# Performance work log

Measured on AMD Instinct MI355X. Metric: run time of the kernel, lower is better.

## Reference

```python
import jax, jax.numpy as jnp
import numpy as np

BATCH, DIM, ORDER = 16384, 1024, 3

def setup_inputs() -> dict:
    key = jax.random.key(0)
    k1, k2, k3 = jax.random.split(key, 3)
    x0 = jax.random.normal(k1, (BATCH, DIM), dtype=jnp.float32)
    # xavier-uniform init scale for w of shape (d, 1): sqrt(6/(d+1))
    limit = float(np.sqrt(6.0 / (DIM + 1)))
    W = jax.random.uniform(k2, (ORDER, DIM), dtype=jnp.float32, minval=-limit, maxval=limit)
    B = jnp.zeros((ORDER, DIM), dtype=jnp.float32)
    return {"x0": x0, "W": W, "B": B}

def reference(x0, W, B):
    # CrossLayer: xi_next = (x0 xi^T) w + b + xi == x0 * (xi . w) + b + xi
    # (outer product followed by matmul with w collapses to a dot-product scale)
    xi = x0
    for l in range(W.shape[0]):  # small fixed number of cross layers
        s = xi @ W[l]                      # [B]  dot(xi, w_l)
        xi = x0 * s[:, None] + B[l] + xi   # [B, D]
    return xi
```

## Files before the change

### kernel.cpp

```cpp
#include <hip/hip_runtime.h>


#define CN_BATCH 16384
#define CN_DIM   1024
#define CN_ORDER 3

__global__ __launch_bounds__(256) void
crossnet_kernel(const float* __restrict__ x0,
                const float* __restrict__ W,
                const float* __restrict__ B,
                float* __restrict__ out)
{
    const int tid  = threadIdx.x;
    const int wave = tid >> 6;
    const int lane = tid & 63;
    const int row  = blockIdx.x * 4 + wave;

    const float* __restrict__ xr = x0 + (size_t)row * CN_DIM;

    float4 x[4], xi[4];
#pragma unroll
    for (int c = 0; c < 4; ++c) {
        x[c]  = *reinterpret_cast<const float4*>(xr + c * 256 + lane * 4);
        xi[c] = x[c];
    }

#pragma unroll
    for (int l = 0; l < CN_ORDER; ++l) {
        const float* __restrict__ wl = W + l * CN_DIM;
        const float* __restrict__ bl = B + l * CN_DIM;

        float4 w[4];
#pragma unroll
        for (int c = 0; c < 4; ++c)
            w[c] = *reinterpret_cast<const float4*>(wl + c * 256 + lane * 4);

        float s = 0.f;
#pragma unroll
        for (int c = 0; c < 4; ++c) {
            s += xi[c].x * w[c].x;
            s += xi[c].y * w[c].y;
            s += xi[c].z * w[c].z;
            s += xi[c].w * w[c].w;
        }

#pragma unroll
        for (int off = 1; off < 64; off <<= 1)
            s += __shfl_xor(s, off, 64);

#pragma unroll
        for (int c = 0; c < 4; ++c) {
            const float4 b = *reinterpret_cast<const float4*>(bl + c * 256 + lane * 4);
            xi[c].x = fmaf(x[c].x, s, xi[c].x + b.x);
            xi[c].y = fmaf(x[c].y, s, xi[c].y + b.y);
            xi[c].z = fmaf(x[c].z, s, xi[c].z + b.z);
            xi[c].w = fmaf(x[c].w, s, xi[c].w + b.w);
        }
    }

    float* __restrict__ orow = out + (size_t)row * CN_DIM;
#pragma unroll
    for (int c = 0; c < 4; ++c)
        *reinterpret_cast<float4*>(orow + c * 256 + lane * 4) = xi[c];
}

extern "C" void kernel_launch(void* const* d_in, const int* in_sizes, int n_in,
                              void* d_out, int out_size, void* d_ws, size_t ws_size,
                              hipStream_t stream)
{
    const float* x0 = (const float*)d_in[0];
    const float* W  = (const float*)d_in[1];
    const float* B  = (const float*)d_in[2];
    float* out      = (float*)d_out;

    const int rows_per_block = 4;
    dim3 grid(CN_BATCH / rows_per_block);
    dim3 block(256);
    crossnet_kernel<<<grid, block, 0, stream>>>(x0, W, B, out);
}
```

Before: 120.5 us.

## Collapse cross layers into one scalar per row and pipeline multiple rows per wave

Uses the fact that every xi is x0 times a scalar plus an accumulated bias. That lets all three dot products be taken against x0 at once, with bias-weight dot products precomputed per block, and the output written as x0*cf + sum(B). Each wave now handles four rows and prefetches the next row while computing the current one. Loads and stores are nontemporal and the launch bound adds a min-blocks hint. The kernel is memory-bound, so the main gains would come from fewer serial reductions, less W/B traffic per row and better overlap, at the cost of higher register use.

```diff
diff --git a/kernel.cpp b/kernel.cpp
--- a/kernel.cpp
+++ b/kernel.cpp
@@ -3,9 +3,14 @@
 
 #define CN_BATCH 16384
 #define CN_DIM   1024
-#define CN_ORDER 3
 
-__global__ __launch_bounds__(256) void
+#define WAVES_PER_BLOCK 4
+#define ROWS_PER_WAVE   4
+#define ROWS_PER_BLOCK  (WAVES_PER_BLOCK * ROWS_PER_WAVE)
+
+typedef float f32x4 __attribute__((ext_vector_type(4)));
+
+__global__ __launch_bounds__(256, 4) void
 crossnet_kernel(const float* __restrict__ x0,
                 const float* __restrict__ W,
                 const float* __restrict__ B,
@@ -14,54 +19,88 @@
     const int tid  = threadIdx.x;
     const int wave = tid >> 6;
     const int lane = tid & 63;
-    const int row  = blockIdx.x * 4 + wave;
+    const int off0 = lane * 4;
 
-    const float* __restrict__ xr = x0 + (size_t)row * CN_DIM;
-
-    float4 x[4], xi[4];
+    f32x4 w0[4], w1[4], w2[4], bs[4];
+    float t1 = 0.f, t2 = 0.f;
 #pragma unroll
     for (int c = 0; c < 4; ++c) {
-        x[c]  = *reinterpret_cast<const float4*>(xr + c * 256 + lane * 4);
-        xi[c] = x[c];
+        const int off = c * 256 + off0;
+        w0[c] = *reinterpret_cast<const f32x4*>(W + 0 * CN_DIM + off);
+        w1[c] = *reinterpret_cast<const f32x4*>(W + 1 * CN_DIM + off);
+        w2[c] = *reinterpret_cast<const f32x4*>(W + 2 * CN_DIM + off);
+        const f32x4 b0 = *reinterpret_cast<const f32x4*>(B + 0 * CN_DIM + off);
+        const f32x4 b1 = *reinterpret_cast<const f32x4*>(B + 1 * CN_DIM + off);
+        const f32x4 b2 = *reinterpret_cast<const f32x4*>(B + 2 * CN_DIM + off);
+        bs[c] = b0 + b1 + b2;
+        t1 = fmaf(b0.x, w1[c].x, t1); t1 = fmaf(b0.y, w1[c].y, t1);
+        t1 = fmaf(b0.z, w1[c].z, t1); t1 = fmaf(b0.w, w1[c].w, t1);
+        t2 = fmaf(b0.x + b1.x, w2[c].x, t2); t2 = fmaf(b0.y + b1.y, w2[c].y, t2);
+        t2 = fmaf(b0.z + b1.z, w2[c].z, t2); t2 = fmaf(b0.w + b1.w, w2[c].w, t2);
+    }
+#pragma unroll
+    for (int o = 1; o < 64; o <<= 1) {
+        t1 += __shfl_xor(t1, o, 64);
+        t2 += __shfl_xor(t2, o, 64);
     }
 
+    const size_t row0 = ((size_t)blockIdx.x * WAVES_PER_BLOCK + wave) * ROWS_PER_WAVE;
+    const float* __restrict__ xr = x0 + row0 * (size_t)CN_DIM;
+
+    f32x4 cur[4], nxt[4];
 #pragma unroll
-    for (int l = 0; l < CN_ORDER; ++l) {
-        const float* __restrict__ wl = W + l * CN_DIM;
-        const float* __restrict__ bl = B + l * CN_DIM;
+    for (int c = 0; c < 4; ++c)
+        cur[c] = __builtin_nontemporal_load(
+            reinterpret_cast<const f32x4*>(xr + c * 256 + off0));
 
-        float4 w[4];
 #pragma unroll
-        for (int c = 0; c < 4; ++c)
-            w[c] = *reinterpret_cast<const float4*>(wl + c * 256 + lane * 4);
+    for (int r = 0; r < ROWS_PER_WAVE; ++r) {
+        if (r + 1 < ROWS_PER_WAVE) {
+#pragma unroll
+            for (int c = 0; c < 4; ++c)
+                nxt[c] = __builtin_nontemporal_load(
+                    reinterpret_cast<const f32x4*>(
+                        xr + (size_t)(r + 1) * CN_DIM + c * 256 + off0));
+        }
 
-        float s = 0.f;
+        float a0 = 0.f, a1 = 0.f, a2 = 0.f;
 #pragma unroll
         for (int c = 0; c < 4; ++c) {
-            s += xi[c].x * w[c].x;
-            s += xi[c].y * w[c].y;
-            s += xi[c].z * w[c].z;
-            s += xi[c].w * w[c].w;
+            a0 = fmaf(cur[c].x, w0[c].x, a0); a0 = fmaf(cur[c].y, w0[c].y, a0);
+            a0 = fmaf(cur[c].z, w0[c].z, a0); a0 = fmaf(cur[c].w, w0[c].w, a0);
+            a1 = fmaf(cur[c].x, w1[c].x, a1); a1 = fmaf(cur[c].y, w1[c].y, a1);
+            a1 = fmaf(cur[c].z, w1[c].z, a1); a1 = fmaf(cur[c].w, w1[c].w, a1);
+            a2 = fmaf(cur[c].x, w2[c].x, a2); a2 = fmaf(cur[c].y, w2[c].y, a2);
+            a2 = fmaf(cur[c].z, w2[c].z, a2); a2 = fmaf(cur[c].w, w2[c].w, a2);
         }
 
 #pragma unroll
-        for (int off = 1; off < 64; off <<= 1)
-            s += __shfl_xor(s, off, 64);
+        for (int o = 1; o < 64; o <<= 1) {
+            a0 += __shfl_xor(a0, o, 64);
+            a1 += __shfl_xor(a1, o, 64);
+            a2 += __shfl_xor(a2, o, 64);
+        }
+
+        const float s0 = a0;
+        const float s1 = fmaf(1.f + s0, a1, t1);
+        const float s2 = fmaf(1.f + s0 + s1, a2, t2);
+        const float cf = 1.f + s0 + s1 + s2;
+
+        float* __restrict__ orow = out + (row0 + (size_t)r) * CN_DIM;
+#pragma unroll
+        for (int c = 0; c < 4; ++c) {
+            f32x4 o;
+            o.x = fmaf(cur[c].x, cf, bs[c].x);
+            o.y = fmaf(cur[c].y, cf, bs[c].y);
+            o.z = fmaf(cur[c].z, cf, bs[c].z);
+            o.w = fmaf(cur[c].w, cf, bs[c].w);
+            __builtin_nontemporal_store(o,
+                reinterpret_cast<f32x4*>(orow + c * 256 + off0));
+        }
 
 #pragma unroll
-        for (int c = 0; c < 4; ++c) {
-            const float4 b = *reinterpret_cast<const float4*>(bl + c * 256 + lane * 4);
-            xi[c].x = fmaf(x[c].x, s, xi[c].x + b.x);
-            xi[c].y = fmaf(x[c].y, s, xi[c].y + b.y);
-            xi[c].z = fmaf(x[c].z, s, xi[c].z + b.z);
-            xi[c].w = fmaf(x[c].w, s, xi[c].w + b.w);
-        }
+        for (int c = 0; c < 4; ++c) cur[c] = nxt[c];
     }
-
-    float* __restrict__ orow = out + (size_t)row * CN_DIM;
-#pragma unroll
-    for (int c = 0; c < 4; ++c)
-        *reinterpret_cast<float4*>(orow + c * 256 + lane * 4) = xi[c];
 }
 
 extern "C" void kernel_launch(void* const* d_in, const int* in_sizes, int n_in,
@@ -73,8 +112,7 @@
     const float* B  = (const float*)d_in[2];
     float* out      = (float*)d_out;
 
-    const int rows_per_block = 4;
-    dim3 grid(CN_BATCH / rows_per_block);
-    dim3 block(256);
+    dim3 grid(CN_BATCH / ROWS_PER_BLOCK);
+    dim3 block(WAVES_PER_BLOCK * 64);
     crossnet_kernel<<<grid, block, 0, stream>>>(x0, W, B, out);
 }
```

Result: slower. 125.5 us (+4.1%).
